# Optimization experiments

Measured on AMD Instinct MI355X. Metric: run time of the kernel, lower is better.

Reference implementation:

```python
import jax, jax.numpy as jnp
import numpy as np
import math

HID_DIM = 1024
NUM_HEADS = 8
QK_DIM = HID_DIM // 8  # 128 total, 16 per head


def setup_inputs() -> dict:
    key = jax.random.key(0)
    ks = jax.random.split(key, 7)
    B, M, C = 4, 2048, HID_DIM
    gain = math.sqrt(2.0)  # calculate_gain('relu')

    def xavier(k, fan_in, fan_out):
        std = gain * math.sqrt(2.0 / (fan_in + fan_out))
        a = math.sqrt(3.0) * std
        return jax.random.uniform(k, (fan_out, fan_in), jnp.float32, -a, a)

    x = jax.random.normal(ks[0], (B, M, C), jnp.float32)
    Wq = xavier(ks[1], C, QK_DIM)   # [out, in] like torch Linear
    Wk = xavier(ks[2], C, QK_DIM)
    Wv = xavier(ks[3], C, C)
    bq = jnp.zeros((QK_DIM,), jnp.float32)
    bk = jnp.zeros((QK_DIM,), jnp.float32)
    bv = jnp.zeros((C,), jnp.float32)
    gamma = jnp.zeros((1,), jnp.float32)
    return {"x": x, "Wq": Wq, "bq": bq, "Wk": Wk, "bk": bk,
            "Wv": Wv, "bv": bv, "gamma": gamma}


def reference(x, Wq, bq, Wk, bk, Wv, bv, gamma):
    B, M, C = x.shape
    H = NUM_HEADS
    dqk = QK_DIM // H   # per-head qk dim = 16
    dv = C // H         # per-head v dim = 128
    q = (x @ Wq.T + bq).reshape(B, M, H, dqk)  # [B,M,H,dqk]
    k = (x @ Wk.T + bk).reshape(B, M, H, dqk)
    v = (x @ Wv.T + bv).reshape(B, M, H, dv)
    scores = jnp.einsum('bmhd,bnhd->bhmn', q, k) / math.sqrt(dqk)
    scores = jnp.where(scores >= 0, scores, 0.2 * scores)  # LeakyReLU(0.2)
    beta = jax.nn.softmax(scores, axis=-1)                 # [B,H,M,M]
    out = jnp.einsum('bhmn,bnhd->bmhd', beta, v).reshape(B, M, C)
    return gamma * out + x
```

## Files before the change

kernel.cpp:

```cpp
#include <hip/hip_runtime.h>
#include <hip/hip_bf16.h>

typedef __bf16 bf16_t;
typedef __bf16 bf16x8 __attribute__((ext_vector_type(8)));
typedef float f32x4 __attribute__((ext_vector_type(4)));
typedef float f32x16 __attribute__((ext_vector_type(16)));

#define MTOT 8192
#define CDIM 1024
#define HEADS 8
#define DV 128
#define QKD 128
#define SEQ 2048
#define QSCALE 0.3606737602222409f

struct alignas(8) B4 { bf16_t a, b, c, d; };

__device__ inline bf16x8 cvt8(float4 a, float4 b) {
    bf16x8 v = { (bf16_t)a.x, (bf16_t)a.y, (bf16_t)a.z, (bf16_t)a.w,
                 (bf16_t)b.x, (bf16_t)b.y, (bf16_t)b.z, (bf16_t)b.w };
    return v;
}

__device__ inline void gl_lds16(const bf16_t* g, bf16_t* l) {
    __builtin_amdgcn_global_load_lds(
        (const __attribute__((address_space(1))) void*)g,
        (__attribute__((address_space(3))) void*)l, 16, 0, 0);
}

__global__ __launch_bounds__(256) void cvt_x(
    const float* __restrict__ src, bf16_t* __restrict__ dst, int n8)
{
    int i = blockIdx.x * blockDim.x + threadIdx.x;
    if (i >= n8) return;
    const float4* s = reinterpret_cast<const float4*>(src) + (size_t)i * 2;
    reinterpret_cast<bf16x8*>(dst)[i] = cvt8(s[0], s[1]);
}

__global__ __launch_bounds__(256) void cvt_w(
    const float* __restrict__ Wq, const float* __restrict__ Wk,
    const float* __restrict__ Wv, bf16_t* __restrict__ Wb)
{
    int i = blockIdx.x * blockDim.x + threadIdx.x;
    const float* src;
    if (i < 16384)       src = Wq + (size_t)i * 8;
    else if (i < 32768)  src = Wk + (size_t)(i - 16384) * 8;
    else                 src = Wv + (size_t)(i - 32768) * 8;
    const float4* s = reinterpret_cast<const float4*>(src);
    reinterpret_cast<bf16x8*>(Wb)[i] = cvt8(s[0], s[1]);
}

__global__ __launch_bounds__(256) void qkv_gemm3(
    const bf16_t* __restrict__ Xb, const bf16_t* __restrict__ Wb,
    const float* __restrict__ bq, const float* __restrict__ bk,
    const float* __restrict__ bv,
    bf16_t* __restrict__ Qw, bf16_t* __restrict__ Kw, bf16_t* __restrict__ Vt)
{
    __shared__ bf16_t As[128][64];
    __shared__ bf16_t Bs[128][64];

    const int tid = threadIdx.x;
    const int w = tid >> 6, l = tid & 63;
    const int c = l & 15, q = l >> 4;
    const int rw = w & 1, cw = w >> 1;
    const int bx = blockIdx.x;
    const int m0 = blockIdx.y * 128;

    const bf16_t* Arow = Xb + (size_t)(m0 + w * 8 + (l >> 3)) * CDIM + (l & 7) * 8;
    const bf16_t* Brow = Wb + (size_t)(bx * 128 + w * 8 + (l >> 3)) * CDIM + (l & 7) * 8;

    f32x4 acc[16] = {};

    for (int k0 = 0; k0 < CDIM; k0 += 64) {
        __syncthreads();
        #pragma unroll
        for (int i = 0; i < 4; ++i) {
            gl_lds16(Arow + k0 + (size_t)i * 32 * CDIM, &As[i * 32 + w * 8][0]);
            gl_lds16(Brow + k0 + (size_t)i * 32 * CDIM, &Bs[i * 32 + w * 8][0]);
        }
        __syncthreads();
        #pragma unroll
        for (int kk = 0; kk < 2; ++kk) {
            bf16x8 af[4], bfr[4];
            #pragma unroll
            for (int mt = 0; mt < 4; ++mt)
                af[mt] = *(const bf16x8*)&As[rw * 64 + mt * 16 + c][kk * 32 + q * 8];
            #pragma unroll
            for (int nt = 0; nt < 4; ++nt)
                bfr[nt] = *(const bf16x8*)&Bs[cw * 64 + nt * 16 + c][kk * 32 + q * 8];
            #pragma unroll
            for (int mt = 0; mt < 4; ++mt)
                #pragma unroll
                for (int nt = 0; nt < 4; ++nt)
                    acc[mt * 4 + nt] = __builtin_amdgcn_mfma_f32_16x16x32_bf16(
                        af[mt], bfr[nt], acc[mt * 4 + nt], 0, 0, 0);
        }
    }

    #pragma unroll
    for (int mt = 0; mt < 4; ++mt)
        #pragma unroll
        for (int nt = 0; nt < 4; ++nt) {
            const int cl = cw * 64 + nt * 16 + c;
            f32x4 a = acc[mt * 4 + nt];
            const int mg = m0 + rw * 64 + mt * 16 + q * 4;
            if (bx == 0) {
                const float bb = bq[cl];
                #pragma unroll
                for (int r = 0; r < 4; ++r)
                    Qw[(size_t)(mg + r) * QKD + cl] = (bf16_t)((a[r] + bb) * QSCALE);
            } else if (bx == 1) {
                const float bb = bk[cl];
                #pragma unroll
                for (int r = 0; r < 4; ++r)
                    Kw[(size_t)(mg + r) * QKD + cl] = (bf16_t)(a[r] + bb);
            } else {
                const int h = bx - 2;
                const float bb = bv[h * DV + cl];
                const int bidx = mg >> 11, ml = mg & 2047;
                B4 v{ (bf16_t)(a[0] + bb), (bf16_t)(a[1] + bb),
                      (bf16_t)(a[2] + bb), (bf16_t)(a[3] + bb) };
                *(B4*)(Vt + ((size_t)(bidx * HEADS + h) * DV + cl) * SEQ + ml) = v;
            }
        }
}

__global__ __launch_bounds__(256, 2) void qkv_gemm2(
    const float* __restrict__ X,
    const float* __restrict__ Wq, const float* __restrict__ bq,
    const float* __restrict__ Wk, const float* __restrict__ bk,
    const float* __restrict__ Wv, const float* __restrict__ bv,
    bf16_t* __restrict__ Qw, bf16_t* __restrict__ Kw, bf16_t* __restrict__ Vt)
{
    __shared__ alignas(16) bf16_t As[128][72];
    __shared__ alignas(16) bf16_t Bs[128][72];

    const int tid  = threadIdx.x;
    const int lane = tid & 63, wave = tid >> 6;
    const int c = lane & 15, q = lane >> 4;
    const int rw = wave & 1, cw = wave >> 1;
    const int m0 = blockIdx.y * 128;
    const int nt_idx = blockIdx.x;

    const float* W; const float* bias;
    if (nt_idx == 0)      { W = Wq; bias = bq; }
    else if (nt_idx == 1) { W = Wk; bias = bk; }
    else { W = Wv + (size_t)(nt_idx - 2) * DV * CDIM; bias = bv + (nt_idx - 2) * DV; }

    const int srow = tid >> 1, sseg = tid & 1;
    const int swr = (srow >> 3) & 3;
    const float* ax = X + (size_t)(m0 + srow) * CDIM + sseg * 32;
    const float* bxp = W + (size_t)srow * CDIM + sseg * 32;

    f32x4 acc[16] = {};

    for (int k0 = 0; k0 < CDIM; k0 += 64) {
        __syncthreads();
        #pragma unroll
        for (int i = 0; i < 4; ++i) {
            const int ph = (sseg * 4 + i) ^ swr;
            *(bf16x8*)&As[srow][ph * 8] = cvt8(*(const float4*)(ax + k0 + i * 8),
                                               *(const float4*)(ax + k0 + i * 8 + 4));
            *(bf16x8*)&Bs[srow][ph * 8] = cvt8(*(const float4*)(bxp + k0 + i * 8),
                                               *(const float4*)(bxp + k0 + i * 8 + 4));
        }
        __syncthreads();
        #pragma unroll
        for (int kk = 0; kk < 2; ++kk) {
            bf16x8 af[4], bfr[4];
            #pragma unroll
            for (int mt = 0; mt < 4; ++mt) {
                const int row = rw * 64 + mt * 16 + c;
                af[mt] = *(const bf16x8*)&As[row][((kk * 4 + q) ^ ((row >> 3) & 3)) * 8];
            }
            #pragma unroll
            for (int nt = 0; nt < 4; ++nt) {
                const int row = cw * 64 + nt * 16 + c;
                bfr[nt] = *(const bf16x8*)&Bs[row][((kk * 4 + q) ^ ((row >> 3) & 3)) * 8];
            }
            #pragma unroll
            for (int mt = 0; mt < 4; ++mt)
                #pragma unroll
                for (int nt = 0; nt < 4; ++nt)
                    acc[mt * 4 + nt] = __builtin_amdgcn_mfma_f32_16x16x32_bf16(
                        af[mt], bfr[nt], acc[mt * 4 + nt], 0, 0, 0);
        }
    }

    #pragma unroll
    for (int mt = 0; mt < 4; ++mt)
        #pragma unroll
        for (int nt = 0; nt < 4; ++nt) {
            const int col = cw * 64 + nt * 16 + c;
            const float bb = bias[col];
            f32x4 a = acc[mt * 4 + nt];
            const int mg = m0 + rw * 64 + mt * 16 + q * 4;
            if (nt_idx == 0) {
                #pragma unroll
                for (int r = 0; r < 4; ++r)
                    Qw[(size_t)(mg + r) * QKD + col] = (bf16_t)((a[r] + bb) * QSCALE);
            } else if (nt_idx == 1) {
                #pragma unroll
                for (int r = 0; r < 4; ++r)
                    Kw[(size_t)(mg + r) * QKD + col] = (bf16_t)(a[r] + bb);
            } else {
                const int h = nt_idx - 2;
                const int bidx = mg >> 11, ml = mg & 2047;
                B4 v{ (bf16_t)(a[0] + bb), (bf16_t)(a[1] + bb),
                      (bf16_t)(a[2] + bb), (bf16_t)(a[3] + bb) };
                *(B4*)(Vt + ((size_t)(bidx * HEADS + h) * DV + col) * SEQ + ml) = v;
            }
        }
}

__global__ __launch_bounds__(256, 2) void attn3(
    const bf16_t* __restrict__ Q, const bf16_t* __restrict__ K,
    const bf16_t* __restrict__ Vt, const float* __restrict__ X,
    const float* __restrict__ gptr, float* __restrict__ out)
{
    __shared__ alignas(16) bf16_t Vs[128][72];
    __shared__ alignas(16) bf16_t Ps[4][32][72];

    const int tid  = threadIdx.x;
    const int lane = tid & 63, wave = tid >> 6;
    const int c5 = lane & 31, q1 = lane >> 5;
    const int bh = blockIdx.y;
    const int b = bh >> 3, h = bh & 7;
    const int mbase = blockIdx.x * 128 + wave * 32;

    const bf16x8 qf = *(const bf16x8*)(
        Q + (size_t)(b * SEQ + mbase + c5) * QKD + h * 16 + q1 * 8);

    float li = 0.f;
    f32x16 o[4] = {};

    const bf16_t* Vhead = Vt + (size_t)(b * HEADS + h) * DV * SEQ;
    const bf16_t* Kbase = K + (size_t)(b * SEQ) * QKD + h * 16;

    const int sdv = tid >> 1, sseg = tid & 1;
    const int swv = (sdv >> 3) & 7;
    const int swp = (c5 >> 3) & 3;

    bf16x8 vreg[4], kreg[2];
    {
        const bf16_t* src = Vhead + (size_t)sdv * SEQ + sseg * 32;
        #pragma unroll
        for (int i = 0; i < 4; ++i) vreg[i] = *(const bf16x8*)(src + i * 8);
        #pragma unroll
        for (int blk = 0; blk < 2; ++blk)
            kreg[blk] = *(const bf16x8*)(Kbase + (size_t)(blk * 32 + c5) * QKD + q1 * 8);
    }

    for (int n0 = 0; n0 < SEQ; n0 += 64) {
        __syncthreads();
        #pragma unroll
        for (int i = 0; i < 4; ++i) {
            const int ph = (sseg * 4 + i) ^ swv;
            *(bf16x8*)&Vs[sdv][ph * 8] = vreg[i];
        }
        __syncthreads();

        const bf16x8 k0f = kreg[0], k1f = kreg[1];
        if (n0 + 64 < SEQ) {
            const bf16_t* src = Vhead + (size_t)sdv * SEQ + n0 + 64 + sseg * 32;
            #pragma unroll
            for (int i = 0; i < 4; ++i) vreg[i] = *(const bf16x8*)(src + i * 8);
            #pragma unroll
            for (int blk = 0; blk < 2; ++blk)
                kreg[blk] = *(const bf16x8*)(
                    Kbase + (size_t)(n0 + 64 + blk * 32 + c5) * QKD + q1 * 8);
        }

        #pragma unroll
        for (int blk = 0; blk < 2; ++blk) {
            f32x16 z = {};
            f32x16 s = __builtin_amdgcn_mfma_f32_32x32x16_bf16(
                blk ? k1f : k0f, qf, z, 0, 0, 0);
            #pragma unroll
            for (int rr = 0; rr < 4; ++rr) {
                float p[4];
                #pragma unroll
                for (int j = 0; j < 4; ++j) {
                    const float sv = s[rr * 4 + j];
                    const float e = __builtin_amdgcn_exp2f(fmaxf(sv, 0.2f * sv));
                    p[j] = e;
                    li += e;
                }
                const int ph = (blk * 4 + rr) ^ swp;
                B4 pv{ (bf16_t)p[0], (bf16_t)p[1], (bf16_t)p[2], (bf16_t)p[3] };
                *(B4*)&Ps[wave][c5][ph * 8 + q1 * 4] = pv;
            }
        }

        #pragma unroll
        for (int kt = 0; kt < 4; ++kt) {
            const int phA = (kt * 2 + q1) ^ swp;
            const bf16x8 pa = *(const bf16x8*)&Ps[wave][c5][phA * 8];
            #pragma unroll
            for (int dvt = 0; dvt < 4; ++dvt) {
                const int dv = dvt * 32 + c5;
                const int phB = (kt * 2 + q1) ^ ((dv >> 3) & 7);
                const bf16x8 vb = *(const bf16x8*)&Vs[dv][phB * 8];
                o[dvt] = __builtin_amdgcn_mfma_f32_32x32x16_bf16(pa, vb, o[dvt], 0, 0, 0);
            }
        }
    }

    li += __shfl_xor(li, 32);
    const float inv = 1.f / li;
    const float g = gptr[0];

    #pragma unroll
    for (int dvt = 0; dvt < 4; ++dvt)
        #pragma unroll
        for (int r = 0; r < 16; ++r) {
            const int row = (r & 3) + 8 * (r >> 2) + 4 * q1;
            const float linv = __shfl(inv, row);
            const size_t idx = (size_t)(b * SEQ + mbase + row) * CDIM
                             + h * DV + dvt * 32 + c5;
            out[idx] = g * (o[dvt][r] * linv) + X[idx];
        }
}

extern "C" void kernel_launch(void* const* d_in, const int* in_sizes, int n_in,
                              void* d_out, int out_size, void* d_ws, size_t ws_size,
                              hipStream_t stream) {
    const float* X  = (const float*)d_in[0];
    const float* Wq = (const float*)d_in[1];
    const float* bq = (const float*)d_in[2];
    const float* Wk = (const float*)d_in[3];
    const float* bk = (const float*)d_in[4];
    const float* Wv = (const float*)d_in[5];
    const float* bv = (const float*)d_in[6];
    const float* g  = (const float*)d_in[7];
    float* out = (float*)d_out;

    dim3 blk(256);
    const size_t big_elems = (size_t)MTOT * CDIM + 1280 * CDIM
                           + (size_t)MTOT * QKD * 2 + (size_t)MTOT * CDIM;
    const size_t big_ws = big_elems * sizeof(bf16_t);

    if (ws_size >= big_ws) {
        bf16_t* Xb = (bf16_t*)d_ws;
        bf16_t* Wb = Xb + (size_t)MTOT * CDIM;
        bf16_t* Qw = Wb + (size_t)1280 * CDIM;
        bf16_t* Kw = Qw + (size_t)MTOT * QKD;
        bf16_t* Vt = Kw + (size_t)MTOT * QKD;

        hipLaunchKernelGGL(cvt_x, dim3(MTOT * CDIM / 8 / 256), blk, 0, stream,
                           X, Xb, MTOT * CDIM / 8);
        hipLaunchKernelGGL(cvt_w, dim3(1280 * CDIM / 8 / 256), blk, 0, stream,
                           Wq, Wk, Wv, Wb);
        hipLaunchKernelGGL(qkv_gemm3, dim3(10, 64), blk, 0, stream,
                           Xb, Wb, bq, bk, bv, Qw, Kw, Vt);
        hipLaunchKernelGGL(attn3, dim3(SEQ / 128, 32), blk, 0, stream,
                           Qw, Kw, Vt, X, g, out);
    } else {
        bf16_t* Qw = (bf16_t*)d_ws;
        bf16_t* Kw = Qw + (size_t)MTOT * QKD;
        bf16_t* Vt = Kw + (size_t)MTOT * QKD;
        hipLaunchKernelGGL(qkv_gemm2, dim3(10, 64), blk, 0, stream,
                           X, Wq, bq, Wk, bk, Wv, bv, Qw, Kw, Vt);
        hipLaunchKernelGGL(attn3, dim3(SEQ / 128, 32), blk, 0, stream,
                           Qw, Kw, Vt, X, g, out);
    }
}
```

Measured before the change: 215.2 us.

## Double-buffer V tile, pass P via register shuffles, remap grid for locality

The attention kernel now double-buffers the V tile in shared memory, so only one barrier is needed per iteration instead of two. The softmax probabilities are repacked into MFMA A-operand layout with cross-half-wave shuffles rather than a round trip through an LDS staging buffer. The launch grid is flattened and remapped so that consecutive blocks belong to different heads of the same batch, which is meant to improve cache reuse of K/V. The cost is double the V shared memory and extra shuffle instructions.

```diff
diff --git a/kernel.cpp b/kernel.cpp
--- a/kernel.cpp
+++ b/kernel.cpp
@@ -5,6 +5,7 @@
 typedef __bf16 bf16x8 __attribute__((ext_vector_type(8)));
 typedef float f32x4 __attribute__((ext_vector_type(4)));
 typedef float f32x16 __attribute__((ext_vector_type(16)));
+typedef unsigned u32x4 __attribute__((ext_vector_type(4)));
 
 #define MTOT 8192
 #define CDIM 1024
@@ -26,6 +27,12 @@
     __builtin_amdgcn_global_load_lds(
         (const __attribute__((address_space(1))) void*)g,
         (__attribute__((address_space(3))) void*)l, 16, 0, 0);
+}
+
+__device__ inline unsigned pk2(float a, float b) {
+    union { bf16_t h[2]; unsigned u; } x;
+    x.h[0] = (bf16_t)a; x.h[1] = (bf16_t)b;
+    return x.u;
 }
 
 __global__ __launch_bounds__(256) void cvt_x(
@@ -213,20 +220,23 @@
         }
 }
 
-__global__ __launch_bounds__(256, 2) void attn3(
+__global__ __launch_bounds__(256, 2) void attn4(
     const bf16_t* __restrict__ Q, const bf16_t* __restrict__ K,
     const bf16_t* __restrict__ Vt, const float* __restrict__ X,
     const float* __restrict__ gptr, float* __restrict__ out)
 {
-    __shared__ alignas(16) bf16_t Vs[128][72];
-    __shared__ alignas(16) bf16_t Ps[4][32][72];
+    __shared__ alignas(16) bf16_t Vs[2][128][72];
 
     const int tid  = threadIdx.x;
     const int lane = tid & 63, wave = tid >> 6;
     const int c5 = lane & 31, q1 = lane >> 5;
-    const int bh = blockIdx.y;
+
+    const int id = blockIdx.x;
+    const int t8 = id >> 3;
+    const int bh = (t8 >> 4) * 8 + (id & 7);
+    const int mtile = t8 & 15;
     const int b = bh >> 3, h = bh & 7;
-    const int mbase = blockIdx.x * 128 + wave * 32;
+    const int mbase = mtile * 128 + wave * 32;
 
     const bf16x8 qf = *(const bf16x8*)(
         Q + (size_t)(b * SEQ + mbase + c5) * QKD + h * 16 + q1 * 8);
@@ -239,7 +249,6 @@
 
     const int sdv = tid >> 1, sseg = tid & 1;
     const int swv = (sdv >> 3) & 7;
-    const int swp = (c5 >> 3) & 3;
 
     bf16x8 vreg[4], kreg[2];
     {
@@ -249,26 +258,25 @@
         #pragma unroll
         for (int blk = 0; blk < 2; ++blk)
             kreg[blk] = *(const bf16x8*)(Kbase + (size_t)(blk * 32 + c5) * QKD + q1 * 8);
-    }
-
-    for (int n0 = 0; n0 < SEQ; n0 += 64) {
-        __syncthreads();
-        #pragma unroll
-        for (int i = 0; i < 4; ++i) {
-            const int ph = (sseg * 4 + i) ^ swv;
-            *(bf16x8*)&Vs[sdv][ph * 8] = vreg[i];
-        }
-        __syncthreads();
-
+        #pragma unroll
+        for (int i = 0; i < 4; ++i)
+            *(bf16x8*)&Vs[0][sdv][(((sseg * 4 + i) ^ swv)) * 8] = vreg[i];
+    }
+    __syncthreads();
+
+    for (int it = 0; it < SEQ / 64; ++it) {
+        const int cur = it & 1, nxt = cur ^ 1;
         const bf16x8 k0f = kreg[0], k1f = kreg[1];
-        if (n0 + 64 < SEQ) {
-            const bf16_t* src = Vhead + (size_t)sdv * SEQ + n0 + 64 + sseg * 32;
+
+        if (it + 1 < SEQ / 64) {
+            const int n1 = (it + 1) * 64;
+            const bf16_t* src = Vhead + (size_t)sdv * SEQ + n1 + sseg * 32;
             #pragma unroll
             for (int i = 0; i < 4; ++i) vreg[i] = *(const bf16x8*)(src + i * 8);
             #pragma unroll
             for (int blk = 0; blk < 2; ++blk)
                 kreg[blk] = *(const bf16x8*)(
-                    Kbase + (size_t)(n0 + 64 + blk * 32 + c5) * QKD + q1 * 8);
+                    Kbase + (size_t)(n1 + blk * 32 + c5) * QKD + q1 * 8);
         }
 
         #pragma unroll
@@ -276,34 +284,51 @@
             f32x16 z = {};
             f32x16 s = __builtin_amdgcn_mfma_f32_32x32x16_bf16(
                 blk ? k1f : k0f, qf, z, 0, 0, 0);
-            #pragma unroll
-            for (int rr = 0; rr < 4; ++rr) {
-                float p[4];
-                #pragma unroll
-                for (int j = 0; j < 4; ++j) {
-                    const float sv = s[rr * 4 + j];
-                    const float e = __builtin_amdgcn_exp2f(fmaxf(sv, 0.2f * sv));
-                    p[j] = e;
-                    li += e;
+
+            float pe[16];
+            #pragma unroll
+            for (int r = 0; r < 16; ++r) {
+                const float sv = s[r];
+                const float e = __builtin_amdgcn_exp2f(fmaxf(sv, 0.2f * sv));
+                pe[r] = e;
+                li += e;
+            }
+
+            unsigned wd[8];
+            #pragma unroll
+            for (int i = 0; i < 8; ++i) wd[i] = pk2(pe[2 * i], pe[2 * i + 1]);
+
+            #pragma unroll
+            for (int kt = 0; kt < 2; ++kt) {
+                const unsigned* wp = wd + kt * 4;
+                const unsigned kA = q1 ? wp[2] : wp[0];
+                const unsigned kB = q1 ? wp[3] : wp[1];
+                const unsigned sA = q1 ? wp[0] : wp[2];
+                const unsigned sB = q1 ? wp[1] : wp[3];
+                const unsigned rA = (unsigned)__shfl_xor((int)sA, 32);
+                const unsigned rB = (unsigned)__shfl_xor((int)sB, 32);
+                u32x4 fw = q1 ? (u32x4){rA, rB, kA, kB}
+                              : (u32x4){kA, kB, rA, rB};
+                bf16x8 pa;
+                __builtin_memcpy(&pa, &fw, 16);
+
+                const int ktg = blk * 2 + kt;
+                #pragma unroll
+                for (int dvt = 0; dvt < 4; ++dvt) {
+                    const int dv = dvt * 32 + c5;
+                    const int phB = (ktg * 2 + q1) ^ ((dv >> 3) & 7);
+                    const bf16x8 vb = *(const bf16x8*)&Vs[cur][dv][phB * 8];
+                    o[dvt] = __builtin_amdgcn_mfma_f32_32x32x16_bf16(pa, vb, o[dvt], 0, 0, 0);
                 }
-                const int ph = (blk * 4 + rr) ^ swp;
-                B4 pv{ (bf16_t)p[0], (bf16_t)p[1], (bf16_t)p[2], (bf16_t)p[3] };
-                *(B4*)&Ps[wave][c5][ph * 8 + q1 * 4] = pv;
-            }
-        }
-
-        #pragma unroll
-        for (int kt = 0; kt < 4; ++kt) {
-            const int phA = (kt * 2 + q1) ^ swp;
-            const bf16x8 pa = *(const bf16x8*)&Ps[wave][c5][phA * 8];
-            #pragma unroll
-            for (int dvt = 0; dvt < 4; ++dvt) {
-                const int dv = dvt * 32 + c5;
-                const int phB = (kt * 2 + q1) ^ ((dv >> 3) & 7);
-                const bf16x8 vb = *(const bf16x8*)&Vs[dv][phB * 8];
-                o[dvt] = __builtin_amdgcn_mfma_f32_32x32x16_bf16(pa, vb, o[dvt], 0, 0, 0);
-            }
-        }
+            }
+        }
+
+        if (it + 1 < SEQ / 64) {
+            #pragma unroll
+            for (int i = 0; i < 4; ++i)
+                *(bf16x8*)&Vs[nxt][sdv][(((sseg * 4 + i) ^ swv)) * 8] = vreg[i];
+        }
+        __syncthreads();
     }
 
     li += __shfl_xor(li, 32);
@@ -353,7 +378,7 @@
                            Wq, Wk, Wv, Wb);
         hipLaunchKernelGGL(qkv_gemm3, dim3(10, 64), blk, 0, stream,
                            Xb, Wb, bq, bk, bv, Qw, Kw, Vt);
-        hipLaunchKernelGGL(attn3, dim3(SEQ / 128, 32), blk, 0, stream,
+        hipLaunchKernelGGL(attn4, dim3(512), blk, 0, stream,
                            Qw, Kw, Vt, X, g, out);
     } else {
         bf16_t* Qw = (bf16_t*)d_ws;
@@ -361,7 +386,7 @@
         bf16_t* Vt = Kw + (size_t)MTOT * QKD;
         hipLaunchKernelGGL(qkv_gemm2, dim3(10, 64), blk, 0, stream,
                            X, Wq, bq, Wk, bk, Wv, bv, Qw, Kw, Vt);
-        hipLaunchKernelGGL(attn3, dim3(SEQ / 128, 32), blk, 0, stream,
+        hipLaunchKernelGGL(attn4, dim3(512), blk, 0, stream,
                            Qw, Kw, Vt, X, g, out);
     }
 }
```

New measurement: 217.2 us. No clear change (+0.9%).
